# Kernel tuning notes

Measured on AMD Instinct MI355X. Metric: run time of the kernel, lower is better.

Reference implementation:

```python
import jax, jax.numpy as jnp
import numpy as np

N = 50000    # num nodes
E = 800000   # num edges
B = 256      # num graphs
AD, BD = 39, 10          # atom / bond feature dims
H, HEADS, HD, L, TD = 128, 4, 32, 3, 128  # hidden, heads, head_dim, layers, time_dim
BN_EPS = 1e-5


def setup_inputs() -> dict:
    key = jax.random.key(0)
    ks = jax.random.split(key, 24)
    g = lambda i, shape: jax.random.normal(ks[i], shape, dtype=jnp.float32) * 0.05
    return {
        "x": jax.random.normal(ks[0], (N, AD), dtype=jnp.float32),
        "edge_index": jax.random.randint(ks[1], (2, E), 0, N),
        "edge_attr": jax.random.normal(ks[2], (E, BD), dtype=jnp.float32),
        "batch": jnp.sort(jax.random.randint(ks[3], (N,), 0, B)),
        "t": jax.random.randint(ks[4], (B,), 0, 1000),
        "atom_W": g(5, (AD, H)), "atom_b": jnp.zeros((H,), jnp.float32),
        "bond_W": g(6, (BD, H)), "bond_b": jnp.zeros((H,), jnp.float32),
        "lin_W": g(7, (L, H, H)), "edge_W": g(8, (L, H, H)),
        "att_src": g(9, (L, HEADS, HD)), "att_dst": g(10, (L, HEADS, HD)),
        "att_edge": g(11, (L, HEADS, HD)), "conv_b": jnp.zeros((L, H), jnp.float32),
        "bn_gamma": jnp.ones((L, H), jnp.float32), "bn_beta": jnp.zeros((L, H), jnp.float32),
        "out_W": g(12, (H, H)), "out_b": jnp.zeros((H,), jnp.float32),
        "time_W1": g(13, (TD, H)), "time_b1": jnp.zeros((H,), jnp.float32),
        "time_W2": g(14, (H, H)), "time_b2": jnp.zeros((H,), jnp.float32),
        "pool_W1": g(15, (H, H)), "pool_b1": jnp.zeros((H,), jnp.float32),
        "pool_W2": g(16, (H, H)), "pool_b2": jnp.zeros((H,), jnp.float32),
        "np_W1": g(17, (2 * H, H)), "np_b1": jnp.zeros((H,), jnp.float32),
        "np_W2": g(18, (H, H)), "np_b2": jnp.zeros((H,), jnp.float32),
        "np_W3": g(19, (H, AD)), "np_b3": jnp.zeros((AD,), jnp.float32),
    }


def _time_embedding(tf):
    half = TD // 2
    freqs = jnp.exp(jnp.arange(half, dtype=jnp.float32) * (-np.log(10000.0) / (half - 1)))
    e = tf[:, None] * freqs[None, :]
    return jnp.concatenate([jnp.sin(e), jnp.cos(e)], axis=-1)


def _gat_layer(h, e_emb, src, dst, W, We, a_src, a_dst, a_edge, bias):
    # PyG GATConv: shared lin for src/dst, edge features modulate attention only.
    xh = (h @ W).reshape(N, HEADS, HD)
    eh = (e_emb @ We).reshape(E, HEADS, HD)
    s_src = jnp.sum(xh * a_src, axis=-1)    # [N, HEADS]
    s_dst = jnp.sum(xh * a_dst, axis=-1)    # [N, HEADS]
    s_edge = jnp.sum(eh * a_edge, axis=-1)  # [E, HEADS]
    alpha = jax.nn.leaky_relu(s_src[src] + s_dst[dst] + s_edge, 0.2)  # [E, HEADS]
    amax = jax.ops.segment_max(alpha, dst, num_segments=N)
    amax = jnp.where(jnp.isfinite(amax), amax, 0.0)
    ea = jnp.exp(alpha - amax[dst])
    denom = jax.ops.segment_sum(ea, dst, num_segments=N)
    w = ea / (denom[dst] + 1e-16)           # segment softmax over incoming edges
    msg = xh[src] * w[:, :, None]           # [E, HEADS, HD]
    return jax.ops.segment_sum(msg, dst, num_segments=N).reshape(N, H) + bias


def reference(x, edge_index, edge_attr, batch, t,
              atom_W, atom_b, bond_W, bond_b,
              lin_W, edge_W, att_src, att_dst, att_edge, conv_b, bn_gamma, bn_beta,
              out_W, out_b, time_W1, time_b1, time_W2, time_b2,
              pool_W1, pool_b1, pool_W2, pool_b2,
              np_W1, np_b1, np_W2, np_b2, np_W3, np_b3):
    src, dst = edge_index[0], edge_index[1]
    # time conditioning
    t_emb = _time_embedding(t.astype(jnp.float32))
    t_emb = jax.nn.silu(t_emb @ time_W1 + time_b1) @ time_W2 + time_b2  # [B, H]
    # GNN backbone
    h = x @ atom_W + atom_b
    e_emb = edge_attr @ bond_W + bond_b
    for i in range(L):
        h_in = h
        h = _gat_layer(h, e_emb, src, dst, lin_W[i], edge_W[i],
                       att_src[i], att_dst[i], att_edge[i], conv_b[i])
        mu = h.mean(axis=0)
        var = h.var(axis=0)
        h = (h - mu) / jnp.sqrt(var + BN_EPS) * bn_gamma[i] + bn_beta[i]
        h = jax.nn.relu(h)
        h = h + h_in  # residual (dropout is eval-mode identity)
    node_features = h @ out_W + out_b  # [N, H]
    # graph mean pool + pooling MLP
    counts = jnp.clip(jax.ops.segment_sum(jnp.ones((N,), h.dtype), batch, num_segments=B), 1.0, None)
    graph = jax.ops.segment_sum(node_features, batch, num_segments=B) / counts[:, None]
    graph = jax.nn.silu(graph @ pool_W1 + pool_b1) @ pool_W2 + pool_b2  # [B, H]
    tg = t_emb + graph
    # per-node noise prediction
    z = jnp.concatenate([node_features, tg[batch]], axis=-1)  # [N, 2H]
    z = jax.nn.silu(z @ np_W1 + np_b1)
    z = jax.nn.silu(z @ np_W2 + np_b2)
    return z @ np_W3 + np_b3  # [N, AD]
```

## Files before the change

kernel.cpp:

```cpp
#include <hip/hip_runtime.h>
#include <hip/hip_fp16.h>
#include <math.h>

#define N_NODES 50000
#define N_EDGES 800000
#define NB 256
#define AD 39
#define BD 10
#define H 128
#define HEADS 4
#define HD 32
#define LAYERS 3
#define TD 128
#define NBUCK 196
#define EPB 4096

typedef _Float16 f16x8 __attribute__((ext_vector_type(8)));
typedef float f32x4 __attribute__((ext_vector_type(4)));

__device__ __forceinline__ float silu_f(float x) { return x / (1.f + __expf(-x)); }

__device__ __forceinline__ void fma_rank1(float acc[8][4], float4 aL, float4 aH, float4 w)
{
    float ar[8] = {aL.x, aL.y, aL.z, aL.w, aH.x, aH.y, aH.z, aH.w};
    float wr[4] = {w.x, w.y, w.z, w.w};
#pragma unroll
    for (int r = 0; r < 8; r++)
#pragma unroll
        for (int j = 0; j < 4; j++) acc[r][j] += ar[r] * wr[j];
}

template<int KT>
__global__ __launch_bounds__(256) void gemm128(
    const float* __restrict__ A, const float* __restrict__ W,
    const float* __restrict__ bias, float* __restrict__ out,
    int Nrows, int ldw)
{
    __shared__ float As[KT * 68];
    const int tid = threadIdx.x;
    const int rowBase = blockIdx.x * 64;

    for (int idx = tid; idx < 64 * KT; idx += 256) {
        int row = idx / KT;
        int k = idx - row * KT;
        int n = rowBase + row;
        As[k * 68 + row] = (n < Nrows) ? A[(size_t)n * KT + k] : 0.f;
    }
    __syncthreads();

    const int c0 = (tid & 31) * 4;
    const int n0 = (tid >> 5) * 8;

    float acc[8][4];
#pragma unroll
    for (int r = 0; r < 8; r++)
#pragma unroll
        for (int j = 0; j < 4; j++) acc[r][j] = 0.f;

    const float* wp = W + c0;
    int k = 0;
    for (; k + 4 <= KT; k += 4) {
        float4 w0 = *(const float4*)&wp[(size_t)(k + 0) * ldw];
        float4 w1 = *(const float4*)&wp[(size_t)(k + 1) * ldw];
        float4 w2 = *(const float4*)&wp[(size_t)(k + 2) * ldw];
        float4 w3 = *(const float4*)&wp[(size_t)(k + 3) * ldw];
        float4 aL0 = *(const float4*)&As[(k + 0) * 68 + n0];
        float4 aH0 = *(const float4*)&As[(k + 0) * 68 + n0 + 4];
        float4 aL1 = *(const float4*)&As[(k + 1) * 68 + n0];
        float4 aH1 = *(const float4*)&As[(k + 1) * 68 + n0 + 4];
        float4 aL2 = *(const float4*)&As[(k + 2) * 68 + n0];
        float4 aH2 = *(const float4*)&As[(k + 2) * 68 + n0 + 4];
        float4 aL3 = *(const float4*)&As[(k + 3) * 68 + n0];
        float4 aH3 = *(const float4*)&As[(k + 3) * 68 + n0 + 4];
        fma_rank1(acc, aL0, aH0, w0);
        fma_rank1(acc, aL1, aH1, w1);
        fma_rank1(acc, aL2, aH2, w2);
        fma_rank1(acc, aL3, aH3, w3);
    }
    for (; k < KT; ++k) {
        float4 w0 = *(const float4*)&wp[(size_t)k * ldw];
        float4 aL = *(const float4*)&As[k * 68 + n0];
        float4 aH = *(const float4*)&As[k * 68 + n0 + 4];
        fma_rank1(acc, aL, aH, w0);
    }

    float4 bv = make_float4(0.f, 0.f, 0.f, 0.f);
    if (bias) bv = *(const float4*)&bias[c0];

#pragma unroll
    for (int r = 0; r < 8; r++) {
        int n = rowBase + n0 + r;
        if (n >= Nrows) break;
        float4 o;
        o.x = acc[r][0] + bv.x;
        o.y = acc[r][1] + bv.y;
        o.z = acc[r][2] + bv.z;
        o.w = acc[r][3] + bv.w;
        *(float4*)&out[(size_t)n * H + c0] = o;
    }
}

__global__ __launch_bounds__(256) void convert_w_frags(
    const float* __restrict__ lin_W, const float* __restrict__ out_W,
    __half* __restrict__ w16)
{
    int tid = blockIdx.x * 256 + threadIdx.x;
    if (tid >= 4 * H * H) return;
    int mat = tid >> 14;
    int rem = tid & 16383;
    int k = rem >> 7;
    int n = rem & 127;
    const float* src = (mat < 3) ? (lin_W + (size_t)mat * H * H) : out_W;
    float v = src[(size_t)k * H + n];
    int ks = k >> 5, kr = k & 31;
    int lane = ((kr >> 3) << 4) | (n & 15);
    int j = kr & 7;
    int nb = n >> 4;
    w16[(size_t)mat * 16384 + (((ks * 8 + nb) * 64 + lane) << 3) + j] = __float2half(v);
}

__global__ __launch_bounds__(256) void convert_np_frags(
    const float* __restrict__ npW1, const float* __restrict__ npW2,
    const float* __restrict__ npW3, __half* __restrict__ wnp)
{
    int tid = blockIdx.x * 256 + threadIdx.x;
    const int TOT12 = 2 * H * H;
    if (tid < TOT12) {
        int mat = tid >> 14;
        int rem = tid & 16383;
        int k = rem >> 7;
        int n = rem & 127;
        const float* src = mat ? npW2 : npW1;
        float v = src[(size_t)k * H + n];
        int ks = k >> 5, kr = k & 31;
        int lane = ((kr >> 3) << 4) | (n & 15);
        int j = kr & 7;
        int nb = n >> 4;
        wnp[(size_t)mat * 16384 + (((ks * 8 + nb) * 64 + lane) << 3) + j] = __float2half(v);
    } else {
        int r = tid - TOT12;
        if (r >= H * 48) return;
        int k = r / 48;
        int n = r - k * 48;
        float v = (n < AD) ? npW3[(size_t)k * AD + n] : 0.f;
        int ks = k >> 5, kr = k & 31;
        int lane = ((kr >> 3) << 4) | (n & 15);
        int j = kr & 7;
        int nb = n >> 4;
        wnp[32768 + (((ks * 3 + nb) * 64 + lane) << 3) + j] = __float2half(v);
    }
}

__global__ __launch_bounds__(256) void gemm_mfma(
    const float* __restrict__ A, const __half* __restrict__ wfrag,
    const float* __restrict__ bias,
    float* __restrict__ out32, __half* __restrict__ out16, int Nrows)
{
    __shared__ __half Ah[64 * 136];
    const int tid = threadIdx.x;
    const int rowBase = blockIdx.x * 64;

    for (int idx = tid; idx < 64 * 32; idx += 256) {
        int row = idx >> 5;
        int kq = (idx & 31) * 4;
        int n = rowBase + row;
        float4 v = make_float4(0.f, 0.f, 0.f, 0.f);
        if (n < Nrows) v = *(const float4*)&A[(size_t)n * H + kq];
        __half2 a = __floats2half2_rn(v.x, v.y);
        __half2 b = __floats2half2_rn(v.z, v.w);
        *(uint2*)&Ah[row * 136 + kq] = make_uint2(*(unsigned*)&a, *(unsigned*)&b);
    }
    __syncthreads();

    const int wave = tid >> 6;
    const int lane = tid & 63;
    const int lrow = lane & 15;
    const int lgrp = lane >> 4;

    f16x8 bf[4][2];
#pragma unroll
    for (int ks = 0; ks < 4; ks++)
#pragma unroll
        for (int nt = 0; nt < 2; nt++) {
            int nb = wave * 2 + nt;
            bf[ks][nt] = *(const f16x8*)&wfrag[(((ks * 8 + nb) * 64 + lane) << 3)];
        }

    f32x4 acc[4][2];
#pragma unroll
    for (int mt = 0; mt < 4; mt++)
#pragma unroll
        for (int nt = 0; nt < 2; nt++) acc[mt][nt] = (f32x4){0.f, 0.f, 0.f, 0.f};

#pragma unroll
    for (int ks = 0; ks < 4; ks++) {
#pragma unroll
        for (int mt = 0; mt < 4; mt++) {
            f16x8 af = *(const f16x8*)&Ah[(mt * 16 + lrow) * 136 + ks * 32 + lgrp * 8];
            acc[mt][0] = __builtin_amdgcn_mfma_f32_16x16x32_f16(af, bf[ks][0], acc[mt][0], 0, 0, 0);
            acc[mt][1] = __builtin_amdgcn_mfma_f32_16x16x32_f16(af, bf[ks][1], acc[mt][1], 0, 0, 0);
        }
    }

#pragma unroll
    for (int mt = 0; mt < 4; mt++) {
#pragma unroll
        for (int nt = 0; nt < 2; nt++) {
            int col = wave * 32 + nt * 16 + lrow;
            float bcol = bias ? bias[col] : 0.f;
#pragma unroll
            for (int reg = 0; reg < 4; reg++) {
                int row = rowBase + mt * 16 + lgrp * 4 + reg;
                if (row < Nrows) {
                    float v = acc[mt][nt][reg] + bcol;
                    if (out16) out16[(size_t)row * H + col] = __float2half(v);
                    else       out32[(size_t)row * H + col] = v;
                }
            }
        }
    }
}

__global__ __launch_bounds__(256) void attn_scores16(
    const __half* __restrict__ xh16, const float* __restrict__ att_src,
    const float* __restrict__ att_dst, float* __restrict__ s_src,
    float* __restrict__ s_dst)
{
    int tid = threadIdx.x;
    int n = blockIdx.x * 2 + (tid >> 7);
    int c = tid & 127;
    float v = __half2float(xh16[(size_t)n * H + c]);
    float as = v * att_src[c];
    float ad = v * att_dst[c];
#pragma unroll
    for (int off = 16; off >= 1; off >>= 1) {
        as += __shfl_xor(as, off, 32);
        ad += __shfl_xor(ad, off, 32);
    }
    if ((c & 31) == 0) {
        s_src[n * 4 + (c >> 5)] = as;
        s_dst[n * 4 + (c >> 5)] = ad;
    }
}

__global__ __launch_bounds__(256) void np_fused_mfma(
    const float* __restrict__ nf, const int* __restrict__ batch,
    const float* __restrict__ tgW, const __half* __restrict__ wnp,
    const float* __restrict__ npb2, const float* __restrict__ npb3,
    float* __restrict__ out, int Nrows)
{
    __shared__ __half Ah[64 * 136];
    const int tid = threadIdx.x;
    const int rowBase = blockIdx.x * 64;

    for (int idx = tid; idx < 64 * 32; idx += 256) {
        int row = idx >> 5;
        int kq = (idx & 31) * 4;
        int n = rowBase + row;
        float4 v = make_float4(0.f, 0.f, 0.f, 0.f);
        if (n < Nrows) v = *(const float4*)&nf[(size_t)n * H + kq];
        __half2 a = __floats2half2_rn(v.x, v.y);
        __half2 b = __floats2half2_rn(v.z, v.w);
        *(uint2*)&Ah[row * 136 + kq] = make_uint2(*(unsigned*)&a, *(unsigned*)&b);
    }
    __syncthreads();

    const int wave = tid >> 6;
    const int lane = tid & 63;
    const int lrow = lane & 15;
    const int lgrp = lane >> 4;

    f32x4 acc[4][2];

    {
        f16x8 bf[4][2];
#pragma unroll
        for (int ks = 0; ks < 4; ks++)
#pragma unroll
            for (int nt = 0; nt < 2; nt++) {
                int nb = wave * 2 + nt;
                bf[ks][nt] = *(const f16x8*)&wnp[(((ks * 8 + nb) * 64 + lane) << 3)];
            }
#pragma unroll
        for (int mt = 0; mt < 4; mt++)
#pragma unroll
            for (int nt = 0; nt < 2; nt++) acc[mt][nt] = (f32x4){0.f, 0.f, 0.f, 0.f};
#pragma unroll
        for (int ks = 0; ks < 4; ks++) {
#pragma unroll
            for (int mt = 0; mt < 4; mt++) {
                f16x8 af = *(const f16x8*)&Ah[(mt * 16 + lrow) * 136 + ks * 32 + lgrp * 8];
                acc[mt][0] = __builtin_amdgcn_mfma_f32_16x16x32_f16(af, bf[ks][0], acc[mt][0], 0, 0, 0);
                acc[mt][1] = __builtin_amdgcn_mfma_f32_16x16x32_f16(af, bf[ks][1], acc[mt][1], 0, 0, 0);
            }
        }
    }
    __syncthreads();

#pragma unroll
    for (int mt = 0; mt < 4; mt++) {
#pragma unroll
        for (int nt = 0; nt < 2; nt++) {
            int col = wave * 32 + nt * 16 + lrow;
#pragma unroll
            for (int reg = 0; reg < 4; reg++) {
                int row = mt * 16 + lgrp * 4 + reg;
                int n = rowBase + row;
                float v = acc[mt][nt][reg];
                if (n < Nrows) v += tgW[(size_t)batch[n] * H + col];
                Ah[row * 136 + col] = __float2half(silu_f(v));
            }
        }
    }
    __syncthreads();

    {
        const __half* w2 = wnp + 16384;
        f16x8 bf[4][2];
#pragma unroll
        for (int ks = 0; ks < 4; ks++)
#pragma unroll
            for (int nt = 0; nt < 2; nt++) {
                int nb = wave * 2 + nt;
                bf[ks][nt] = *(const f16x8*)&w2[(((ks * 8 + nb) * 64 + lane) << 3)];
            }
#pragma unroll
        for (int mt = 0; mt < 4; mt++)
#pragma unroll
            for (int nt = 0; nt < 2; nt++) acc[mt][nt] = (f32x4){0.f, 0.f, 0.f, 0.f};
#pragma unroll
        for (int ks = 0; ks < 4; ks++) {
#pragma unroll
            for (int mt = 0; mt < 4; mt++) {
                f16x8 af = *(const f16x8*)&Ah[(mt * 16 + lrow) * 136 + ks * 32 + lgrp * 8];
                acc[mt][0] = __builtin_amdgcn_mfma_f32_16x16x32_f16(af, bf[ks][0], acc[mt][0], 0, 0, 0);
                acc[mt][1] = __builtin_amdgcn_mfma_f32_16x16x32_f16(af, bf[ks][1], acc[mt][1], 0, 0, 0);
            }
        }
    }
    __syncthreads();

#pragma unroll
    for (int mt = 0; mt < 4; mt++) {
#pragma unroll
        for (int nt = 0; nt < 2; nt++) {
            int col = wave * 32 + nt * 16 + lrow;
            float b2 = npb2[col];
#pragma unroll
            for (int reg = 0; reg < 4; reg++) {
                int row = mt * 16 + lgrp * 4 + reg;
                Ah[row * 136 + col] = __float2half(silu_f(acc[mt][nt][reg] + b2));
            }
        }
    }
    __syncthreads();

    {
        const __half* w3 = wnp + 32768;
        f32x4 acc3[3];
#pragma unroll
        for (int nt = 0; nt < 3; nt++) acc3[nt] = (f32x4){0.f, 0.f, 0.f, 0.f};
#pragma unroll
        for (int ks = 0; ks < 4; ks++) {
            f16x8 af = *(const f16x8*)&Ah[(wave * 16 + lrow) * 136 + ks * 32 + lgrp * 8];
#pragma unroll
            for (int nt = 0; nt < 3; nt++) {
                f16x8 bf = *(const f16x8*)&w3[(((ks * 3 + nt) * 64 + lane) << 3)];
                acc3[nt] = __builtin_amdgcn_mfma_f32_16x16x32_f16(af, bf, acc3[nt], 0, 0, 0);
            }
        }
#pragma unroll
        for (int nt = 0; nt < 3; nt++) {
            int col = nt * 16 + lrow;
            if (col < AD) {
                float b3 = npb3[col];
#pragma unroll
                for (int reg = 0; reg < 4; reg++) {
                    int row = rowBase + wave * 16 + lgrp * 4 + reg;
                    if (row < Nrows) out[(size_t)row * AD + col] = acc3[nt][reg] + b3;
                }
            }
        }
    }
}

__global__ __launch_bounds__(256) void precompute_small(
    const float* __restrict__ edge_W, const float* __restrict__ att_edge,
    const float* __restrict__ bond_W, const float* __restrict__ bond_b,
    float* __restrict__ mc)
{
    __shared__ float bl[LAYERS][H][4];
    int tid = threadIdx.x;
    for (int task = tid; task < LAYERS * H; task += 256) {
        int l = task / H, k = task % H;
#pragma unroll
        for (int hh = 0; hh < 4; hh++) {
            float s = 0.f;
            for (int d = 0; d < HD; d++)
                s += edge_W[(size_t)l * H * H + k * H + hh * HD + d] *
                     att_edge[l * H + hh * HD + d];
            bl[l][k][hh] = s;
        }
    }
    __syncthreads();
    if (tid < LAYERS * BD * 4) {
        int l = tid / (BD * 4), r = tid % (BD * 4), j = r / 4, hh = r % 4;
        float s = 0.f;
        for (int k = 0; k < H; k++) s += bond_W[j * H + k] * bl[l][k][hh];
        mc[l * 44 + j * 4 + hh] = s;
    }
    if (tid >= 128 && tid < 128 + LAYERS * 4) {
        int r = tid - 128, l = r / 4, hh = r % 4;
        float s = 0.f;
        for (int k = 0; k < H; k++) s += bond_b[k] * bl[l][k][hh];
        mc[l * 44 + 40 + hh] = s;
    }
}

__global__ __launch_bounds__(128) void time_embed(
    const int* __restrict__ t,
    const float* __restrict__ W1, const float* __restrict__ b1,
    const float* __restrict__ W2, const float* __restrict__ b2,
    float* __restrict__ t_emb)
{
    int g = blockIdx.x, c = threadIdx.x;
    float tf = (float)t[g];
    __shared__ float emb[TD], z[H];
    int k = c & 63;
    float f = __expf(-9.210340371976184f * (float)k / 63.0f);
    float e = tf * f;
    emb[c] = (c < 64) ? sinf(e) : cosf(e);
    __syncthreads();
    float a1 = b1[c];
    for (int kk = 0; kk < TD; kk++) a1 += emb[kk] * W1[kk * H + c];
    z[c] = silu_f(a1);
    __syncthreads();
    float a2 = b2[c];
    for (int kk = 0; kk < H; kk++) a2 += z[kk] * W2[kk * H + c];
    t_emb[g * H + c] = a2;
}

__global__ __launch_bounds__(256) void hist_dst(const int* __restrict__ edge_index,
                                                int* __restrict__ deg)
{
    int e = blockIdx.x * 256 + threadIdx.x;
    if (e < N_EDGES) atomicAdd(&deg[edge_index[N_EDGES + e]], 1);
}

__global__ __launch_bounds__(320) void gptr_bsearch(const int* __restrict__ batch,
                                                    int* __restrict__ gptr)
{
    int g = threadIdx.x;
    if (g > NB) return;
    int lo = 0, hi = N_NODES;
    while (lo < hi) {
        int mid = (lo + hi) >> 1;
        if (batch[mid] < g) lo = mid + 1; else hi = mid;
    }
    gptr[g] = lo;
}

__global__ __launch_bounds__(256) void scan_part(const int* __restrict__ cnt,
                                                 int* __restrict__ bsum, int n)
{
    int tid = threadIdx.x;
    int i0 = blockIdx.x * 1024 + tid * 4;
    int s = 0;
#pragma unroll
    for (int j = 0; j < 4; j++) if (i0 + j < n) s += cnt[i0 + j];
    __shared__ int red[256];
    red[tid] = s;
    __syncthreads();
    for (int off = 128; off >= 1; off >>= 1) {
        if (tid < off) red[tid] += red[tid + off];
        __syncthreads();
    }
    if (tid == 0) bsum[blockIdx.x] = red[0];
}

__global__ __launch_bounds__(256) void scan_tops(const int* __restrict__ bsum,
                                                 int* __restrict__ boff, int G,
                                                 int* __restrict__ total)
{
    int tid = threadIdx.x;
    int v = (tid < G) ? bsum[tid] : 0;
    __shared__ int ps[256];
    ps[tid] = v;
    __syncthreads();
    for (int off = 1; off < 256; off <<= 1) {
        int t = (tid >= off) ? ps[tid - off] : 0;
        __syncthreads();
        ps[tid] += t;
        __syncthreads();
    }
    if (tid < G) boff[tid] = ps[tid] - v;
    if (tid == 255) *total = ps[255];
}

__global__ __launch_bounds__(256) void scan_final(const int* __restrict__ cnt,
                                                  const int* __restrict__ boff,
                                                  int* __restrict__ ptr, int n)
{
    int tid = threadIdx.x;
    int i0 = blockIdx.x * 1024 + tid * 4;
    int v[4];
#pragma unroll
    for (int j = 0; j < 4; j++) v[j] = (i0 + j < n) ? cnt[i0 + j] : 0;
    int s = v[0] + v[1] + v[2] + v[3];
    __shared__ int ps[256];
    ps[tid] = s;
    __syncthreads();
    for (int off = 1; off < 256; off <<= 1) {
        int t = (tid >= off) ? ps[tid - off] : 0;
        __syncthreads();
        ps[tid] += t;
        __syncthreads();
    }
    int run = boff[blockIdx.x] + ps[tid] - s;
#pragma unroll
    for (int j = 0; j < 4; j++) {
        if (i0 + j < n) { ptr[i0 + j] = run; run += v[j]; }
    }
}

__global__ __launch_bounds__(256) void init_gcur(const int* __restrict__ csr_ptr,
                                                 int* __restrict__ gcur)
{
    int b = threadIdx.x;
    if (b < NBUCK) gcur[b] = csr_ptr[min(b << 8, N_NODES)];
}

__global__ __launch_bounds__(256) void bucket_scatter_a(
    const int* __restrict__ edge_index, int* __restrict__ gcur,
    int4* __restrict__ tmp)
{
    __shared__ int cnt[NBUCK], cbase[NBUCK], cur[NBUCK];
    const int tid = threadIdx.x;
    const int e0 = blockIdx.x * EPB;
    for (int i = tid; i < NBUCK; i += 256) { cnt[i] = 0; cur[i] = 0; }
    __syncthreads();
    for (int i = 0; i < EPB; i += 256) {
        int e = e0 + i + tid;
        if (e < N_EDGES) atomicAdd(&cnt[edge_index[N_EDGES + e] >> 8], 1);
    }
    __syncthreads();
    for (int i = tid; i < NBUCK; i += 256)
        if (cnt[i] > 0) cbase[i] = atomicAdd(&gcur[i], cnt[i]);
    __syncthreads();
    for (int i = 0; i < EPB; i += 256) {
        int e = e0 + i + tid;
        if (e < N_EDGES) {
            int s = edge_index[e];
            int d = edge_index[N_EDGES + e];
            int b = d >> 8;
            int off = atomicAdd(&cur[b], 1);
            tmp[cbase[b] + off] = make_int4(s, e, d, 0);
        }
    }
}

__global__ __launch_bounds__(256) void bucket_scatter_b(
    const int4* __restrict__ tmp, const int* __restrict__ csr_ptr,
    int2* __restrict__ csr_se)
{
    __shared__ int lcur[256];
    const int b = blockIdx.x;
    const int n0 = b << 8;
    const int tid = threadIdx.x;
    lcur[tid] = 0;
    __syncthreads();
    int start = csr_ptr[n0];
    int end   = csr_ptr[min(n0 + 256, N_NODES)];
    for (int p = start + tid; p < end; p += 256) {
        int4 q = tmp[p];
        int pos = atomicAdd(&lcur[q.z - n0], 1);
        csr_se[csr_ptr[q.z] + pos] = make_int2(q.x, q.y);
    }
}

__global__ __launch_bounds__(256) void ase_csr(
    const int2* __restrict__ csr_se, const float* __restrict__ edge_attr,
    const float* __restrict__ sS, const float* __restrict__ mc_l,
    __half* __restrict__ ase)
{
    __shared__ float Ml[BD * 4], cl[4];
    int tid = threadIdx.x;
    if (tid < 40) Ml[tid] = mc_l[tid];
    if (tid >= 40 && tid < 44) cl[tid - 40] = mc_l[tid];
    __syncthreads();
    int p = blockIdx.x * 256 + tid;
    if (p >= N_EDGES) return;
    int2 q = csr_se[p];
    float4 ss = *(const float4*)&sS[q.x * 4];
    float s0 = cl[0] + ss.x, s1 = cl[1] + ss.y;
    float s2 = cl[2] + ss.z, s3 = cl[3] + ss.w;
    const float* ea = &edge_attr[(size_t)q.y * BD];
#pragma unroll
    for (int j = 0; j < BD; j++) {
        float x = ea[j];
        s0 += x * Ml[j * 4 + 0]; s1 += x * Ml[j * 4 + 1];
        s2 += x * Ml[j * 4 + 2]; s3 += x * Ml[j * 4 + 3];
    }
    __half2 h01 = __floats2half2_rn(s0, s1);
    __half2 h23 = __floats2half2_rn(s2, s3);
    uint2 u = make_uint2(*(const unsigned*)&h01, *(const unsigned*)&h23);
    *(uint2*)&ase[(size_t)p * 4] = u;
}

__global__ __launch_bounds__(256) void gat_agg_full(
    const __half* __restrict__ xh16, const __half* __restrict__ ase,
    const int* __restrict__ csr_ptr, const int2* __restrict__ csr_se,
    const float* __restrict__ sD, const float* __restrict__ conv_b_l,
    __half* __restrict__ agg)
{
    int n = (blockIdx.x * 256 + threadIdx.x) >> 6;
    if (n >= N_NODES) return;
    int lane = threadIdx.x & 63;
    int c0 = lane * 2;
    int hd = lane >> 4;
    int start = csr_ptr[n], end = csr_ptr[n + 1];
    float sDn = sD[n * 4 + hd];

    float m_run = -1e30f, d_run = 0.f;
    float acc0 = 0.f, acc1 = 0.f;

    for (int base = start; base < end; base += 64) {
        int cnt = min(64, end - base);
        int s_l = (lane < cnt) ? csr_se[base + lane].x : 0;

        float a_t[4], e_t[4];
        float m_blk = -1e30f;
#pragma unroll
        for (int t = 0; t < 4; t++) {
            int i = (lane & 15) + t * 16;
            float a = -1e30f;
            if (i < cnt) {
                a = __half2float(ase[(size_t)(base + i) * 4 + hd]) + sDn;
                a = (a >= 0.f) ? a : 0.2f * a;
            }
            a_t[t] = a;
            m_blk = fmaxf(m_blk, a);
        }
#pragma unroll
        for (int off = 8; off >= 1; off >>= 1)
            m_blk = fmaxf(m_blk, __shfl_xor(m_blk, off, 16));
        float m_new = fmaxf(m_run, m_blk);
        float rescale = __expf(m_run - m_new);
        float dsum = 0.f;
#pragma unroll
        for (int t = 0; t < 4; t++) {
            e_t[t] = __expf(a_t[t] - m_new);
            dsum += e_t[t];
        }
#pragma unroll
        for (int off = 8; off >= 1; off >>= 1)
            dsum += __shfl_xor(dsum, off, 16);
        d_run = d_run * rescale + dsum;
        acc0 *= rescale;
        acc1 *= rescale;

        int srcb = lane & 48;
#pragma unroll
        for (int t = 0; t < 4; t++) {
            int rem = cnt - t * 16;
            if (rem <= 0) break;
            int lim = min(16, (rem + 3) & ~3);
            for (int i2 = 0; i2 < lim; i2 += 4) {
                int i = t * 16 + i2;
                int s0 = __shfl(s_l, i + 0), s1 = __shfl(s_l, i + 1);
                int s2 = __shfl(s_l, i + 2), s3 = __shfl(s_l, i + 3);
                float w0 = __shfl(e_t[t], srcb | (i2 + 0));
                float w1 = __shfl(e_t[t], srcb | (i2 + 1));
                float w2 = __shfl(e_t[t], srcb | (i2 + 2));
                float w3 = __shfl(e_t[t], srcb | (i2 + 3));
                float2 x0 = __half22float2(*(const __half2*)&xh16[(size_t)s0 * H + c0]);
                float2 x1 = __half22float2(*(const __half2*)&xh16[(size_t)s1 * H + c0]);
                float2 x2 = __half22float2(*(const __half2*)&xh16[(size_t)s2 * H + c0]);
                float2 x3 = __half22float2(*(const __half2*)&xh16[(size_t)s3 * H + c0]);
                acc0 += x0.x * w0 + x1.x * w1 + x2.x * w2 + x3.x * w3;
                acc1 += x0.y * w0 + x1.y * w1 + x2.y * w2 + x3.y * w3;
            }
        }
        m_run = m_new;
    }
    float inv = 1.f / (d_run + 1e-16f);
    __half2 o = __floats2half2_rn(acc0 * inv + conv_b_l[c0],
                                  acc1 * inv + conv_b_l[c0 + 1]);
    *(__half2*)&agg[(size_t)n * H + c0] = o;
}

__global__ __launch_bounds__(256) void bn_partial_f(const __half* __restrict__ agg,
                                                    float* __restrict__ part)
{
    const int PER = (N_NODES + 511) / 512;
    __shared__ float red[2][8][128];
    int b = blockIdx.x;
    int cg = threadIdx.x & 31;
    int rs = threadIdx.x >> 5;
    int c4 = cg * 4;
    int s = b * PER, e = min(N_NODES, s + PER);
    float s0 = 0.f, s1 = 0.f, s2 = 0.f, s3 = 0.f;
    float q0 = 0.f, q1 = 0.f, q2 = 0.f, q3 = 0.f;
    for (int n = s + rs; n < e; n += 8) {
        uint2 u = *(const uint2*)&agg[(size_t)n * H + c4];
        float2 lo = __half22float2(*(__half2*)&u.x);
        float2 hi = __half22float2(*(__half2*)&u.y);
        s0 += lo.x; q0 += lo.x * lo.x;
        s1 += lo.y; q1 += lo.y * lo.y;
        s2 += hi.x; q2 += hi.x * hi.x;
        s3 += hi.y; q3 += hi.y * hi.y;
    }
    *(float4*)&red[0][rs][c4] = make_float4(s0, s1, s2, s3);
    *(float4*)&red[1][rs][c4] = make_float4(q0, q1, q2, q3);
    __syncthreads();
    if (threadIdx.x < 128) {
        int c = threadIdx.x;
        float sum = 0.f, sq = 0.f;
#pragma unroll
        for (int r = 0; r < 8; r++) { sum += red[0][r][c]; sq += red[1][r][c]; }
        part[b * H + c] = sum;
        part[512 * H + b * H + c] = sq;
    }
}

__global__ __launch_bounds__(256) void bn_finish_f(const float* __restrict__ part,
                                                   const float* __restrict__ gamma,
                                                   const float* __restrict__ beta,
                                                   float* __restrict__ scale,
                                                   float* __restrict__ shift)
{
    __shared__ double red[2][2][128];
    int c = threadIdx.x & 127;
    int g = threadIdx.x >> 7;
    double s = 0.0, q = 0.0;
    for (int b = g * 256; b < (g + 1) * 256; b++) {
        s += (double)part[b * H + c];
        q += (double)part[512 * H + b * H + c];
    }
    red[0][g][c] = s;
    red[1][g][c] = q;
    __syncthreads();
    if (g == 0) {
        s = red[0][0][c] + red[0][1][c];
        q = red[1][0][c] + red[1][1][c];
        float mu = (float)(s / N_NODES);
        float var = (float)(q / N_NODES) - mu * mu;
        float rstd = rsqrtf(var + 1e-5f);
        float sc = gamma[c] * rstd;
        scale[c] = sc;
        shift[c] = beta[c] - mu * sc;
    }
}

__global__ __launch_bounds__(256) void bn_apply_f(const __half* __restrict__ agg,
                                                  const float* __restrict__ scale,
                                                  const float* __restrict__ shift,
                                                  float* __restrict__ h)
{
    int i = blockIdx.x * 256 + threadIdx.x;
    if (i >= N_NODES * H / 4) return;
    int n = i >> 5;
    int c0 = (i & 31) * 4;
    uint2 u = *(const uint2*)&agg[(size_t)n * H + c0];
    __half2 h01 = *(__half2*)&u.x;
    __half2 h23 = *(__half2*)&u.y;
    float2 v01 = __half22float2(h01);
    float2 v23 = __half22float2(h23);
    float4 sc = *(const float4*)&scale[c0];
    float4 sh = *(const float4*)&shift[c0];
    float* hp = &h[(size_t)n * H + c0];
    float4 hv = *(const float4*)hp;
    float4 o;
    o.x = fmaxf(v01.x * sc.x + sh.x, 0.f) + hv.x;
    o.y = fmaxf(v01.y * sc.y + sh.y, 0.f) + hv.y;
    o.z = fmaxf(v23.x * sc.z + sh.z, 0.f) + hv.z;
    o.w = fmaxf(v23.y * sc.w + sh.w, 0.f) + hv.w;
    *(float4*)hp = o;
}

__global__ __launch_bounds__(128) void pool_partial(
    const float* __restrict__ nf, const int* __restrict__ gptr,
    float* __restrict__ pprt)
{
    int g = blockIdx.x >> 2;
    int q = blockIdx.x & 3;
    int c = threadIdx.x;
    int s = gptr[g], e = gptr[g + 1];
    int qlen = (e - s + 3) >> 2;
    int qs = s + q * qlen;
    int qe = min(e, qs + qlen);
    float sum = 0.f;
    for (int n = qs; n < qe; n++) sum += nf[(size_t)n * H + c];
    pprt[((size_t)g * 4 + q) * H + c] = sum;
}

__global__ __launch_bounds__(512) void graph_head_mlp(
    const int* __restrict__ gptr, const float* __restrict__ pprt,
    const float* __restrict__ t_emb,
    const float* __restrict__ pW1, const float* __restrict__ pb1,
    const float* __restrict__ pW2, const float* __restrict__ pb2,
    const float* __restrict__ npW1, const float* __restrict__ npb1,
    float* __restrict__ tgW)
{
    int g = blockIdx.x;
    int c = threadIdx.x & 127;
    int q = threadIdx.x >> 7;
    __shared__ float row[H], z[H];
    __shared__ float red[4][H];

    int s = gptr[g], e = gptr[g + 1];
    float cf = (e - s > 0) ? (float)(e - s) : 1.f;
    if (q == 0) {
        row[c] = (pprt[((size_t)g * 4 + 0) * H + c] +
                  pprt[((size_t)g * 4 + 1) * H + c] +
                  pprt[((size_t)g * 4 + 2) * H + c] +
                  pprt[((size_t)g * 4 + 3) * H + c]) / cf;
    }
    __syncthreads();

    float p = 0.f;
#pragma unroll 8
    for (int k = q * 32; k < q * 32 + 32; k++) p += row[k] * pW1[k * H + c];
    red[q][c] = p;
    __syncthreads();
    if (q == 0) z[c] = silu_f(red[0][c] + red[1][c] + red[2][c] + red[3][c] + pb1[c]);
    __syncthreads();

    p = 0.f;
#pragma unroll 8
    for (int k = q * 32; k < q * 32 + 32; k++) p += z[k] * pW2[k * H + c];
    red[q][c] = p;
    __syncthreads();
    if (q == 0) row[c] = red[0][c] + red[1][c] + red[2][c] + red[3][c] + pb2[c]
                         + t_emb[g * H + c];
    __syncthreads();

    p = 0.f;
#pragma unroll 8
    for (int k = q * 32; k < q * 32 + 32; k++)
        p += row[k] * npW1[(size_t)(128 + k) * H + c];
    red[q][c] = p;
    __syncthreads();
    if (q == 0) tgW[g * H + c] = red[0][c] + red[1][c] + red[2][c] + red[3][c] + npb1[c];
}

extern "C" void kernel_launch(void* const* d_in, const int* in_sizes, int n_in,
                              void* d_out, int out_size, void* d_ws, size_t ws_size,
                              hipStream_t stream)
{
    const float* x          = (const float*)d_in[0];
    const int*   edge_index = (const int*)d_in[1];
    const float* edge_attr  = (const float*)d_in[2];
    const int*   batch      = (const int*)d_in[3];
    const int*   t          = (const int*)d_in[4];
    const float* atom_W     = (const float*)d_in[5];
    const float* atom_b     = (const float*)d_in[6];
    const float* bond_W     = (const float*)d_in[7];
    const float* bond_b     = (const float*)d_in[8];
    const float* lin_W      = (const float*)d_in[9];
    const float* edge_W     = (const float*)d_in[10];
    const float* att_src    = (const float*)d_in[11];
    const float* att_dst    = (const float*)d_in[12];
    const float* att_edge   = (const float*)d_in[13];
    const float* conv_b     = (const float*)d_in[14];
    const float* bn_gamma   = (const float*)d_in[15];
    const float* bn_beta    = (const float*)d_in[16];
    const float* out_W      = (const float*)d_in[17];
    const float* out_b      = (const float*)d_in[18];
    const float* time_W1    = (const float*)d_in[19];
    const float* time_b1    = (const float*)d_in[20];
    const float* time_W2    = (const float*)d_in[21];
    const float* time_b2    = (const float*)d_in[22];
    const float* pool_W1    = (const float*)d_in[23];
    const float* pool_b1    = (const float*)d_in[24];
    const float* pool_W2    = (const float*)d_in[25];
    const float* pool_b2    = (const float*)d_in[26];
    const float* np_W1      = (const float*)d_in[27];
    const float* np_b1      = (const float*)d_in[28];
    const float* np_W2      = (const float*)d_in[29];
    const float* np_b2      = (const float*)d_in[30];
    const float* np_W3      = (const float*)d_in[31];
    const float* np_b3      = (const float*)d_in[32];

    const size_t OFF_H     = 0;
    const size_t OFF_XH    = 6400000;
    const size_t OFF_AGG   = 12800000;
    const size_t OFF_ASE   = 16000000;
    const size_t OFF_SD    = 17600000;
    const size_t OFF_TEMB  = 17800000;
    const size_t OFF_TGW   = 17832768;
    const size_t OFF_MC    = 17865536;
    const size_t OFF_BNSC  = 17865792;
    const size_t OFF_BNSH  = 17865920;
    const size_t OFF_PART  = 17866048;
    const size_t REQ_FLOATS = 17898816;
    const size_t REQ_BYTES  = REQ_FLOATS * 4;

    if (ws_size < REQ_BYTES) {
        hipMemsetAsync(d_out, 0, (size_t)out_size * sizeof(float), stream);
        return;
    }

    float* fws    = (float*)d_ws;
    float* h      = fws + OFF_H;
    float* xh     = fws + OFF_XH;
    __half* xh16  = (__half*)(fws + OFF_XH);
    int4*  etmp   = (int4*)(fws + OFF_XH);
    __half* agg   = (__half*)(fws + OFF_AGG);
    __half* ase   = (__half*)(fws + OFF_ASE);
    float* sD     = fws + OFF_SD;
    float* t_emb  = fws + OFF_TEMB;
    float* tgW    = fws + OFF_TGW;
    float* mc     = fws + OFF_MC;
    float* bnsc   = fws + OFF_BNSC;
    float* bnsh   = fws + OFF_BNSH;
    float* part   = fws + OFF_PART;
    float* pprt   = fws + OFF_AGG;
    __half* wnp   = (__half*)part;

    int* ib       = (int*)d_out;
    int* csr_ptr  = ib;
    int2* csr_se  = (int2*)(ib + 50016);
    int* deg      = ib + 1650016;
    int* gcur     = deg;
    int* gptr     = ib + 1700032;
    int* bsum     = ib + 1700292;
    int* boff     = ib + 1700356;
    float* sS     = (float*)d_out + 1700420;
    float* bnpart = sS;
    __half* w16   = (__half*)((float*)d_out + 1900420);

    hipMemsetAsync(deg, 0, N_NODES * sizeof(int), stream);

    precompute_small<<<1, 256, 0, stream>>>(edge_W, att_edge, bond_W, bond_b, mc);
    time_embed<<<NB, 128, 0, stream>>>(t, time_W1, time_b1, time_W2, time_b2, t_emb);
    gptr_bsearch<<<1, 320, 0, stream>>>(batch, gptr);
    convert_w_frags<<<(4 * H * H + 255) / 256, 256, 0, stream>>>(lin_W, out_W, w16);

    hist_dst<<<(N_EDGES + 255) / 256, 256, 0, stream>>>(edge_index, deg);

    const int GSN = (N_NODES + 1023) / 1024;
    scan_part<<<GSN, 256, 0, stream>>>(deg, bsum, N_NODES);
    scan_tops<<<1, 256, 0, stream>>>(bsum, boff, GSN, &csr_ptr[N_NODES]);
    scan_final<<<GSN, 256, 0, stream>>>(deg, boff, csr_ptr, N_NODES);

    init_gcur<<<1, 256, 0, stream>>>(csr_ptr, gcur);
    bucket_scatter_a<<<(N_EDGES + EPB - 1) / EPB, 256, 0, stream>>>(
        edge_index, gcur, etmp);
    bucket_scatter_b<<<NBUCK, 256, 0, stream>>>(etmp, csr_ptr, csr_se);

    const int GB = (N_NODES + 63) / 64;
    const int GE = (N_EDGES + 255) / 256;

    gemm128<AD><<<GB, 256, 0, stream>>>(x, atom_W, atom_b, h, N_NODES, H);

    for (int l = 0; l < LAYERS; l++) {
        gemm_mfma<<<GB, 256, 0, stream>>>(h, w16 + (size_t)l * 16384, nullptr,
                                          nullptr, xh16, N_NODES);
        attn_scores16<<<N_NODES / 2, 256, 0, stream>>>(xh16, att_src + l * H,
                                                       att_dst + l * H, sS, sD);
        ase_csr<<<GE, 256, 0, stream>>>(csr_se, edge_attr, sS, mc + l * 44, ase);
        gat_agg_full<<<N_NODES / 4, 256, 0, stream>>>(
            xh16, ase, csr_ptr, csr_se, sD, conv_b + l * H, agg);
        bn_partial_f<<<512, 256, 0, stream>>>(agg, bnpart);
        bn_finish_f<<<1, 256, 0, stream>>>(bnpart, bn_gamma + l * H,
                                           bn_beta + l * H, bnsc, bnsh);
        bn_apply_f<<<(N_NODES * H / 4 + 255) / 256, 256, 0, stream>>>(
            agg, bnsc, bnsh, h);
    }

    convert_np_frags<<<(2 * H * H + H * 48 + 255) / 256, 256, 0, stream>>>(
        np_W1, np_W2, np_W3, wnp);

    gemm_mfma<<<GB, 256, 0, stream>>>(h, w16 + (size_t)3 * 16384, out_b,
                                      xh, nullptr, N_NODES);

    pool_partial<<<NB * 4, 128, 0, stream>>>(xh, gptr, pprt);
    graph_head_mlp<<<NB, 512, 0, stream>>>(gptr, pprt, t_emb, pool_W1, pool_b1,
                                           pool_W2, pool_b2, np_W1, np_b1, tgW);

    np_fused_mfma<<<GB, 256, 0, stream>>>(xh, batch, tgW, wnp, np_b2, np_b3,
                                          (float*)d_out, N_NODES);
}
```

Baseline: 519.6 us.

## Fuse BN-apply into next GEMM prologue and attention scores into GEMM epilogue

The batch-norm apply, ReLU and residual step is folded into the load stage of the following MFMA GEMM, which writes the updated h back while staging it into shared memory. The per-head attention score dot products are computed in the GEMM epilogue with 16-lane shuffles, so the separate attn_scores16 and bn_apply_f kernels are removed. This saves two launches per layer and one full read of xh16 and agg. In exchange the GEMM load phase does more global traffic and the epilogue carries extra shuffle reductions.

```diff
diff --git a/kernel.cpp b/kernel.cpp
--- a/kernel.cpp
+++ b/kernel.cpp
@@ -151,10 +151,14 @@
     }
 }
 
-__global__ __launch_bounds__(256) void gemm_mfma(
-    const float* __restrict__ A, const __half* __restrict__ wfrag,
-    const float* __restrict__ bias,
-    float* __restrict__ out32, __half* __restrict__ out16, int Nrows)
+__global__ __launch_bounds__(256) void gemm_mfma_bn(
+    const float* __restrict__ A,
+    const __half* __restrict__ agg, const float* __restrict__ scale,
+    const float* __restrict__ shift, float* __restrict__ hio,
+    const __half* __restrict__ wfrag, const float* __restrict__ bias,
+    float* __restrict__ out32, __half* __restrict__ out16,
+    const float* __restrict__ attS, const float* __restrict__ attD,
+    float* __restrict__ sS, float* __restrict__ sD, int Nrows)
 {
     __shared__ __half Ah[64 * 136];
     const int tid = threadIdx.x;
@@ -165,7 +169,23 @@
         int kq = (idx & 31) * 4;
         int n = rowBase + row;
         float4 v = make_float4(0.f, 0.f, 0.f, 0.f);
-        if (n < Nrows) v = *(const float4*)&A[(size_t)n * H + kq];
+        if (n < Nrows) {
+            if (agg) {
+                uint2 u = *(const uint2*)&agg[(size_t)n * H + kq];
+                float2 lo = __half22float2(*(__half2*)&u.x);
+                float2 hi = __half22float2(*(__half2*)&u.y);
+                float4 sc = *(const float4*)&scale[kq];
+                float4 sh = *(const float4*)&shift[kq];
+                float4 hv = *(const float4*)&hio[(size_t)n * H + kq];
+                v.x = fmaxf(lo.x * sc.x + sh.x, 0.f) + hv.x;
+                v.y = fmaxf(lo.y * sc.y + sh.y, 0.f) + hv.y;
+                v.z = fmaxf(hi.x * sc.z + sh.z, 0.f) + hv.z;
+                v.w = fmaxf(hi.y * sc.w + sh.w, 0.f) + hv.w;
+                *(float4*)&hio[(size_t)n * H + kq] = v;
+            } else {
+                v = *(const float4*)&A[(size_t)n * H + kq];
+            }
+        }
         __half2 a = __floats2half2_rn(v.x, v.y);
         __half2 b = __floats2half2_rn(v.z, v.w);
         *(uint2*)&Ah[row * 136 + kq] = make_uint2(*(unsigned*)&a, *(unsigned*)&b);
@@ -202,44 +222,46 @@
         }
     }
 
+    const int col0 = wave * 32 + lrow;
+    const int col1 = col0 + 16;
+    float b0 = bias ? bias[col0] : 0.f;
+    float b1 = bias ? bias[col1] : 0.f;
+    float aS0 = 0.f, aS1 = 0.f, aD0 = 0.f, aD1 = 0.f;
+    if (sS) {
+        aS0 = attS[col0]; aS1 = attS[col1];
+        aD0 = attD[col0]; aD1 = attD[col1];
+    }
+
 #pragma unroll
     for (int mt = 0; mt < 4; mt++) {
 #pragma unroll
-        for (int nt = 0; nt < 2; nt++) {
-            int col = wave * 32 + nt * 16 + lrow;
-            float bcol = bias ? bias[col] : 0.f;
-#pragma unroll
-            for (int reg = 0; reg < 4; reg++) {
-                int row = rowBase + mt * 16 + lgrp * 4 + reg;
-                if (row < Nrows) {
-                    float v = acc[mt][nt][reg] + bcol;
-                    if (out16) out16[(size_t)row * H + col] = __float2half(v);
-                    else       out32[(size_t)row * H + col] = v;
+        for (int reg = 0; reg < 4; reg++) {
+            int row = rowBase + mt * 16 + lgrp * 4 + reg;
+            float v0 = acc[mt][0][reg] + b0;
+            float v1 = acc[mt][1][reg] + b1;
+            if (row < Nrows) {
+                if (out16) {
+                    out16[(size_t)row * H + col0] = __float2half(v0);
+                    out16[(size_t)row * H + col1] = __float2half(v1);
+                } else {
+                    out32[(size_t)row * H + col0] = v0;
+                    out32[(size_t)row * H + col1] = v1;
                 }
             }
-        }
-    }
-}
-
-__global__ __launch_bounds__(256) void attn_scores16(
-    const __half* __restrict__ xh16, const float* __restrict__ att_src,
-    const float* __restrict__ att_dst, float* __restrict__ s_src,
-    float* __restrict__ s_dst)
-{
-    int tid = threadIdx.x;
-    int n = blockIdx.x * 2 + (tid >> 7);
-    int c = tid & 127;
-    float v = __half2float(xh16[(size_t)n * H + c]);
-    float as = v * att_src[c];
-    float ad = v * att_dst[c];
-#pragma unroll
-    for (int off = 16; off >= 1; off >>= 1) {
-        as += __shfl_xor(as, off, 32);
-        ad += __shfl_xor(ad, off, 32);
-    }
-    if ((c & 31) == 0) {
-        s_src[n * 4 + (c >> 5)] = as;
-        s_dst[n * 4 + (c >> 5)] = ad;
+            if (sS) {
+                float ps = v0 * aS0 + v1 * aS1;
+                float pd = v0 * aD0 + v1 * aD1;
+#pragma unroll
+                for (int off = 8; off >= 1; off >>= 1) {
+                    ps += __shfl_xor(ps, off, 16);
+                    pd += __shfl_xor(pd, off, 16);
+                }
+                if (lrow == 0 && row < Nrows) {
+                    sS[row * 4 + wave] = ps;
+                    sD[row * 4 + wave] = pd;
+                }
+            }
+        }
     }
 }
 
@@ -750,32 +772,6 @@
         scale[c] = sc;
         shift[c] = beta[c] - mu * sc;
     }
-}
-
-__global__ __launch_bounds__(256) void bn_apply_f(const __half* __restrict__ agg,
-                                                  const float* __restrict__ scale,
-                                                  const float* __restrict__ shift,
-                                                  float* __restrict__ h)
-{
-    int i = blockIdx.x * 256 + threadIdx.x;
-    if (i >= N_NODES * H / 4) return;
-    int n = i >> 5;
-    int c0 = (i & 31) * 4;
-    uint2 u = *(const uint2*)&agg[(size_t)n * H + c0];
-    __half2 h01 = *(__half2*)&u.x;
-    __half2 h23 = *(__half2*)&u.y;
-    float2 v01 = __half22float2(h01);
-    float2 v23 = __half22float2(h23);
-    float4 sc = *(const float4*)&scale[c0];
-    float4 sh = *(const float4*)&shift[c0];
-    float* hp = &h[(size_t)n * H + c0];
-    float4 hv = *(const float4*)hp;
-    float4 o;
-    o.x = fmaxf(v01.x * sc.x + sh.x, 0.f) + hv.x;
-    o.y = fmaxf(v01.y * sc.y + sh.y, 0.f) + hv.y;
-    o.z = fmaxf(v23.x * sc.z + sh.z, 0.f) + hv.z;
-    o.w = fmaxf(v23.y * sc.w + sh.w, 0.f) + hv.w;
-    *(float4*)hp = o;
 }
 
 __global__ __launch_bounds__(128) void pool_partial(
@@ -955,25 +951,28 @@
     gemm128<AD><<<GB, 256, 0, stream>>>(x, atom_W, atom_b, h, N_NODES, H);
 
     for (int l = 0; l < LAYERS; l++) {
-        gemm_mfma<<<GB, 256, 0, stream>>>(h, w16 + (size_t)l * 16384, nullptr,
-                                          nullptr, xh16, N_NODES);
-        attn_scores16<<<N_NODES / 2, 256, 0, stream>>>(xh16, att_src + l * H,
-                                                       att_dst + l * H, sS, sD);
+        gemm_mfma_bn<<<GB, 256, 0, stream>>>(
+            (l == 0) ? h : nullptr,
+            (l == 0) ? nullptr : agg, bnsc, bnsh, h,
+            w16 + (size_t)l * 16384, nullptr,
+            nullptr, xh16,
+            att_src + l * H, att_dst + l * H, sS, sD, N_NODES);
         ase_csr<<<GE, 256, 0, stream>>>(csr_se, edge_attr, sS, mc + l * 44, ase);
         gat_agg_full<<<N_NODES / 4, 256, 0, stream>>>(
             xh16, ase, csr_ptr, csr_se, sD, conv_b + l * H, agg);
         bn_partial_f<<<512, 256, 0, stream>>>(agg, bnpart);
         bn_finish_f<<<1, 256, 0, stream>>>(bnpart, bn_gamma + l * H,
                                            bn_beta + l * H, bnsc, bnsh);
-        bn_apply_f<<<(N_NODES * H / 4 + 255) / 256, 256, 0, stream>>>(
-            agg, bnsc, bnsh, h);
     }
 
     convert_np_frags<<<(2 * H * H + H * 48 + 255) / 256, 256, 0, stream>>>(
         np_W1, np_W2, np_W3, wnp);
 
-    gemm_mfma<<<GB, 256, 0, stream>>>(h, w16 + (size_t)3 * 16384, out_b,
-                                      xh, nullptr, N_NODES);
+    gemm_mfma_bn<<<GB, 256, 0, stream>>>(
+        nullptr, agg, bnsc, bnsh, h,
+        w16 + (size_t)3 * 16384, out_b,
+        xh, nullptr,
+        nullptr, nullptr, nullptr, nullptr, N_NODES);
 
     pool_partial<<<NB * 4, 128, 0, stream>>>(xh, gptr, pprt);
     graph_head_mlp<<<NB, 512, 0, stream>>>(gptr, pprt, t_emb, pool_W1, pool_b1,
```

After: 471.6 us. -9.2%, faster.
